# Kernel optimization log

Measured on AMD Instinct MI355X. Metric: run time of the kernel, lower is better.

Reference implementation:

```python
import jax, jax.numpy as jnp
import numpy as np

N_NODES = 100000
N_EDGES = 20000
NNZ = 1600000


def _hconv(x, node_idx, edge_idx, W, b):
    # PyG HypergraphConv (no attention): out = D^-1 H (B^-1 H^T (x W)) + b
    xw = x @ W  # [N, F_out]
    ones = jnp.ones((node_idx.shape[0],), dtype=x.dtype)
    Bdeg = jax.ops.segment_sum(ones, edge_idx, num_segments=N_EDGES)
    Binv = jnp.where(Bdeg > 0, 1.0 / Bdeg, 0.0)
    # node -> hyperedge aggregation
    e = jax.ops.segment_sum(xw[node_idx], edge_idx, num_segments=N_EDGES)
    e = e * Binv[:, None]
    Ddeg = jax.ops.segment_sum(ones, node_idx, num_segments=N_NODES)
    Dinv = jnp.where(Ddeg > 0, 1.0 / Ddeg, 0.0)
    # hyperedge -> node aggregation
    out = jax.ops.segment_sum(e[edge_idx], node_idx, num_segments=N_NODES)
    return out * Dinv[:, None] + b


def setup_inputs() -> dict:
    key = jax.random.key(0)
    ks = jax.random.split(key, 12)
    x = jax.random.normal(ks[0], (N_NODES, 300), dtype=jnp.float32)
    node_idx = jax.random.randint(ks[1], (NNZ,), 0, N_NODES)
    edge_idx = jax.random.randint(ks[2], (NNZ,), 0, N_EDGES)
    hyper_edge_index = jnp.stack([node_idx, edge_idx], axis=0)
    def lin(kw, kb, fi, fo):
        s = 1.0 / np.sqrt(fi)
        W = jax.random.uniform(kw, (fi, fo), jnp.float32, -s, s)
        b = jax.random.uniform(kb, (fo,), jnp.float32, -s, s)
        return W, b
    W1, b1 = lin(ks[3], ks[4], 300, 256)
    W2, b2 = lin(ks[5], ks[6], 256, 256)
    W3, b3 = lin(ks[7], ks[8], 256, 128)
    attn_W, attn_b = lin(ks[9], ks[10], 128, 1)
    return {"x": x, "hyper_edge_index": hyper_edge_index,
            "W1": W1, "b1": b1, "W2": W2, "b2": b2,
            "W3": W3, "b3": b3, "attn_W": attn_W, "attn_b": attn_b}


def reference(x, hyper_edge_index, W1, b1, W2, b2, W3, b3, attn_W, attn_b):
    node_idx = hyper_edge_index[0]
    edge_idx = hyper_edge_index[1]
    h = jax.nn.leaky_relu(_hconv(x, node_idx, edge_idx, W1, b1), negative_slope=0.01)
    # dropout is identity at inference
    h = jax.nn.leaky_relu(_hconv(h, node_idx, edge_idx, W2, b2), negative_slope=0.01)
    h = _hconv(h, node_idx, edge_idx, W3, b3)  # [N, 128]
    # attention pooling over all nodes (softmax along dim 0)
    logits = h @ attn_W + attn_b  # [N, 1]
    attn = jax.nn.softmax(logits, axis=0)
    return jnp.sum(attn * h, axis=0)  # [128]
```

## Files before the change

kernel.cpp:

```cpp
#include <hip/hip_runtime.h>
#include <hip/hip_bf16.h>
#include <string.h>

#define N_NODES 100000
#define N_EDGES 20000
#define NNZ     1600000

#define CHUNK   8192
#define NBE     157
#define NBN     391
#define NBLK_BIN ((NNZ + CHUNK - 1) / CHUNK)


__device__ __forceinline__ unsigned short f2bf(float f) {
    unsigned int u = __float_as_uint(f);
    unsigned int r = (u + 0x7fffu + ((u >> 16) & 1u)) >> 16;
    return (unsigned short)r;
}
__device__ __forceinline__ float bflo(unsigned int v) { return __uint_as_float(v << 16); }
__device__ __forceinline__ float bfhi(unsigned int v) { return __uint_as_float(v & 0xffff0000u); }
__device__ __forceinline__ unsigned int packbf(float lo, float hi) {
    return ((unsigned int)f2bf(hi) << 16) | (unsigned int)f2bf(lo);
}

__device__ __forceinline__ void async_copy16(const void* g, void* l) {
    __builtin_amdgcn_global_load_lds((const __attribute__((address_space(1))) void*)g,
                                     (__attribute__((address_space(3))) void*)l, 16, 0, 0);
}

typedef __attribute__((ext_vector_type(8))) short bf16x8;
typedef __attribute__((ext_vector_type(4))) float f32x4;


__global__ __launch_bounds__(256)
void hist_buckets(const int* __restrict__ node_idx, const int* __restrict__ edge_idx,
                  int* __restrict__ bcntE, int* __restrict__ bcntN) {
    __shared__ int hE[NBE];
    __shared__ int hN[NBN];
    int t = threadIdx.x;
    for (int i = t; i < NBE; i += 256) hE[i] = 0;
    for (int i = t; i < NBN; i += 256) hN[i] = 0;
    __syncthreads();
    long base = (long)blockIdx.x * CHUNK;
    #pragma unroll 4
    for (int k = 0; k < CHUNK / 256; k++) {
        long i = base + t + k * 256;
        if (i < NNZ) {
            atomicAdd(&hE[edge_idx[i] >> 7], 1);
            atomicAdd(&hN[node_idx[i] >> 8], 1);
        }
    }
    __syncthreads();
    for (int i = t; i < NBE; i += 256) if (hE[i]) atomicAdd(&bcntE[i], hE[i]);
    for (int i = t; i < NBN; i += 256) if (hN[i]) atomicAdd(&bcntN[i], hN[i]);
}

__global__ __launch_bounds__(512)
void small_scan(const int* __restrict__ cnt, int n,
                int* __restrict__ base, int* __restrict__ cursor) {
    __shared__ int tmp[512];
    int t = threadIdx.x;
    int v = (t < n) ? cnt[t] : 0;
    tmp[t] = v; __syncthreads();
    for (int s = 1; s < 512; s <<= 1) {
        int x = (t >= s) ? tmp[t - s] : 0;
        __syncthreads();
        tmp[t] += x;
        __syncthreads();
    }
    if (t < n) { int e = tmp[t] - v; base[t] = e; cursor[t] = e; }
    if (t == 0) base[n] = tmp[511];
}

__global__ __launch_bounds__(256)
void bin_pass(const int* __restrict__ key_idx, const int* __restrict__ val_idx,
              int kshift, int bshift, int nbuck,
              int* __restrict__ cursor, unsigned int* __restrict__ staged) {
    __shared__ int hist[512];
    __shared__ int gstart[512];
    int t = threadIdx.x;
    for (int i = t; i < nbuck; i += 256) hist[i] = 0;
    __syncthreads();
    long base = (long)blockIdx.x * CHUNK;
    for (int k = 0; k < CHUNK / 256; k++) {
        long i = base + t + k * 256;
        if (i < NNZ) atomicAdd(&hist[key_idx[i] >> bshift], 1);
    }
    __syncthreads();
    for (int i = t; i < nbuck; i += 256)
        gstart[i] = hist[i] ? atomicAdd(&cursor[i], hist[i]) : 0;
    __syncthreads();
    for (int i = t; i < nbuck; i += 256) hist[i] = 0;
    __syncthreads();
    for (int k = 0; k < CHUNK / 256; k++) {
        long i = base + t + k * 256;
        if (i < NNZ) {
            int key = key_idx[i], val = val_idx[i];
            int b = key >> bshift;
            int pos = gstart[b] + atomicAdd(&hist[b], 1);
            staged[pos] = ((unsigned int)key << kshift) | (unsigned int)val;
        }
    }
}

__global__ __launch_bounds__(256)
void build_csr(const unsigned int* __restrict__ staged, const int* __restrict__ bbase,
               int kshift, int bshift, int nkey,
               int* __restrict__ off, float* __restrict__ inv, int* __restrict__ csr) {
    __shared__ int cnt[256];
    __shared__ int cur[256];
    int b = blockIdx.x, t = threadIdx.x;
    int kpb = 1 << bshift;
    int key0 = b << bshift;
    unsigned int vmask = (1u << kshift) - 1u;
    if (t < kpb) cnt[t] = 0;
    __syncthreads();
    int s = bbase[b], e = bbase[b + 1];
    for (int j = s + t; j < e; j += 256)
        atomicAdd(&cnt[(int)(staged[j] >> kshift) - key0], 1);
    __syncthreads();
    int v = (t < kpb) ? cnt[t] : 0;
    cur[t] = v; __syncthreads();
    for (int st = 1; st < 256; st <<= 1) {
        int x = (t >= st) ? cur[t - st] : 0;
        __syncthreads();
        cur[t] += x;
        __syncthreads();
    }
    int excl = cur[t] - v;
    __syncthreads();
    if (t < kpb) {
        int key = key0 + t;
        if (key < nkey) {
            off[key] = s + excl;
            inv[key] = (v > 0) ? 1.0f / (float)v : 0.0f;
        }
        cur[t] = excl;
    }
    __syncthreads();
    for (int j = s + t; j < e; j += 256) {
        unsigned int pk = staged[j];
        int k = (int)(pk >> kshift) - key0;
        int pos = s + atomicAdd(&cur[k], 1);
        csr[pos] = (int)(pk & vmask);
    }
    if (b == 0 && t == 0) off[nkey] = NNZ;
}


__global__ void convert_pad_x(const float* __restrict__ x, unsigned short* __restrict__ xb) {
    int idx = blockIdx.x * 256 + threadIdx.x;
    if (idx < N_NODES * 320) {
        int r = idx / 320, k = idx - r * 320;
        xb[idx] = (k < 300) ? f2bf(x[(size_t)r * 300 + k]) : (unsigned short)0;
    }
}

__global__ void transpose_w(const float* __restrict__ W, unsigned short* __restrict__ Wt,
                            int K, int N, int Kp) {
    int n = blockIdx.x;
    for (int k = threadIdx.x; k < Kp; k += 256)
        Wt[(size_t)n * Kp + k] = (k < K) ? f2bf(W[(size_t)k * N + n]) : (unsigned short)0;
}


__global__ __launch_bounds__(256)
void gemm_bf16(const unsigned short* __restrict__ A,
               const unsigned short* __restrict__ Bt,
               unsigned short* __restrict__ C,
               int M, int Kp, int N) {
    __shared__ unsigned short As[128 * 32];
    __shared__ unsigned short Bs[128 * 32];
    int tid = threadIdx.x;
    int lane = tid & 63;
    int w = tid >> 6;
    int row0 = blockIdx.x * 128;
    int col0 = blockIdx.y * 128;
    int wm = w & 1, wn = w >> 1;

    f32x4 acc[4][4];
    #pragma unroll
    for (int i = 0; i < 4; i++)
        #pragma unroll
        for (int j = 0; j < 4; j++) acc[i][j] = (f32x4){0.f, 0.f, 0.f, 0.f};

    int sr = lane >> 2;
    int sc = lane & 3;

    for (int k0 = 0; k0 < Kp; k0 += 32) {
        #pragma unroll
        for (int c = 0; c < 2; c++) {
            int r = w * 32 + c * 16 + sr;
            int gr = row0 + r; if (gr >= M) gr = M - 1;
            const unsigned short* g = A + (size_t)gr * Kp + k0 + sc * 8;
            async_copy16(g, (void*)(As + (w * 32 + c * 16) * 32));
        }
        #pragma unroll
        for (int c = 0; c < 2; c++) {
            int r = w * 32 + c * 16 + sr;
            const unsigned short* g = Bt + (size_t)(col0 + r) * Kp + k0 + sc * 8;
            async_copy16(g, (void*)(Bs + (w * 32 + c * 16) * 32));
        }
        __syncthreads();

        bf16x8 a[4], b[4];
        #pragma unroll
        for (int i = 0; i < 4; i++)
            a[i] = *(const bf16x8*)(As + (wm * 64 + i * 16 + (lane & 15)) * 32 + (lane >> 4) * 8);
        #pragma unroll
        for (int j = 0; j < 4; j++)
            b[j] = *(const bf16x8*)(Bs + (wn * 64 + j * 16 + (lane & 15)) * 32 + (lane >> 4) * 8);
        #pragma unroll
        for (int i = 0; i < 4; i++)
            #pragma unroll
            for (int j = 0; j < 4; j++)
                acc[i][j] = __builtin_amdgcn_mfma_f32_16x16x32_bf16(a[i], b[j], acc[i][j], 0, 0, 0);
        __syncthreads();
    }

    int crow = (lane >> 4) * 4;
    int ccol = lane & 15;
    #pragma unroll
    for (int i = 0; i < 4; i++)
        #pragma unroll
        for (int r = 0; r < 4; r++) {
            int gr = row0 + wm * 64 + i * 16 + crow + r;
            if (gr < M) {
                #pragma unroll
                for (int j = 0; j < 4; j++) {
                    int gc = col0 + wn * 64 + j * 16 + ccol;
                    C[(size_t)gr * N + gc] = f2bf(acc[i][j][r]);
                }
            }
        }
}


__global__ __launch_bounds__(256)
void edge_agg256(const unsigned short* __restrict__ X, const int* __restrict__ off,
                 const int* __restrict__ csr, const float* __restrict__ inv,
                 unsigned short* __restrict__ E) {
    int wv = threadIdx.x >> 6, lane = threadIdx.x & 63;
    int seg = blockIdx.x * 4 + wv;
    if (seg >= N_EDGES) return;
    int s = off[seg], t = off[seg + 1];
    const uint2* Xp = (const uint2*)X;
    float a0 = 0.f, a1 = 0.f, a2 = 0.f, a3 = 0.f;
    int j = s;
    for (; j + 3 < t; j += 4) {
        uint2 v[4];
        #pragma unroll
        for (int q = 0; q < 4; q++) v[q] = Xp[(size_t)csr[j + q] * 64 + lane];
        #pragma unroll
        for (int q = 0; q < 4; q++) {
            a0 += bflo(v[q].x); a1 += bfhi(v[q].x);
            a2 += bflo(v[q].y); a3 += bfhi(v[q].y);
        }
    }
    for (; j < t; j++) {
        uint2 v = Xp[(size_t)csr[j] * 64 + lane];
        a0 += bflo(v.x); a1 += bfhi(v.x); a2 += bflo(v.y); a3 += bfhi(v.y);
    }
    float bi = inv[seg];
    uint2 o; o.x = packbf(a0 * bi, a1 * bi); o.y = packbf(a2 * bi, a3 * bi);
    ((uint2*)E)[(size_t)seg * 64 + lane] = o;
}

__global__ __launch_bounds__(256)
void node_agg256(const unsigned short* __restrict__ Eb, const int* __restrict__ off,
                 const int* __restrict__ csr, const float* __restrict__ inv,
                 const float* __restrict__ bias, unsigned short* __restrict__ outB) {
    int wv = threadIdx.x >> 6, lane = threadIdx.x & 63;
    int seg = blockIdx.x * 4 + wv;
    if (seg >= N_NODES) return;
    int s = off[seg], t = off[seg + 1];
    const uint2* Ep = (const uint2*)Eb;
    float a0 = 0.f, a1 = 0.f, a2 = 0.f, a3 = 0.f;
    int j = s;
    for (; j + 3 < t; j += 4) {
        uint2 v[4];
        #pragma unroll
        for (int q = 0; q < 4; q++) v[q] = Ep[(size_t)csr[j + q] * 64 + lane];
        #pragma unroll
        for (int q = 0; q < 4; q++) {
            a0 += bflo(v[q].x); a1 += bfhi(v[q].x);
            a2 += bflo(v[q].y); a3 += bfhi(v[q].y);
        }
    }
    for (; j < t; j++) {
        uint2 v = Ep[(size_t)csr[j] * 64 + lane];
        a0 += bflo(v.x); a1 += bfhi(v.x); a2 += bflo(v.y); a3 += bfhi(v.y);
    }
    float di = inv[seg];
    float4 b4 = ((const float4*)bias)[lane];
    float o0 = a0 * di + b4.x, o1 = a1 * di + b4.y;
    float o2 = a2 * di + b4.z, o3 = a3 * di + b4.w;
    o0 = (o0 > 0.f) ? o0 : 0.01f * o0;
    o1 = (o1 > 0.f) ? o1 : 0.01f * o1;
    o2 = (o2 > 0.f) ? o2 : 0.01f * o2;
    o3 = (o3 > 0.f) ? o3 : 0.01f * o3;
    uint2 o; o.x = packbf(o0, o1); o.y = packbf(o2, o3);
    ((uint2*)outB)[(size_t)seg * 64 + lane] = o;
}

__global__ __launch_bounds__(256)
void edge_agg128(const unsigned short* __restrict__ X, const int* __restrict__ off,
                 const int* __restrict__ csr, const float* __restrict__ inv,
                 unsigned short* __restrict__ E) {
    int wv = threadIdx.x >> 6, lane = threadIdx.x & 63;
    int seg = blockIdx.x * 4 + wv;
    if (seg >= N_EDGES) return;
    int s = off[seg], t = off[seg + 1];
    const unsigned int* Xp = (const unsigned int*)X;
    float a0 = 0.f, a1 = 0.f;
    int j = s;
    for (; j + 7 < t; j += 8) {
        unsigned int v[8];
        #pragma unroll
        for (int q = 0; q < 8; q++) v[q] = Xp[(size_t)csr[j + q] * 64 + lane];
        #pragma unroll
        for (int q = 0; q < 8; q++) { a0 += bflo(v[q]); a1 += bfhi(v[q]); }
    }
    for (; j < t; j++) {
        unsigned int v = Xp[(size_t)csr[j] * 64 + lane];
        a0 += bflo(v); a1 += bfhi(v);
    }
    float bi = inv[seg];
    ((unsigned int*)E)[(size_t)seg * 64 + lane] = packbf(a0 * bi, a1 * bi);
}

__global__ __launch_bounds__(256)
void node_agg128f(const unsigned short* __restrict__ Eb, const int* __restrict__ off,
                  const int* __restrict__ csr, const float* __restrict__ inv,
                  const float* __restrict__ bias, float* __restrict__ outF) {
    int wv = threadIdx.x >> 6, lane = threadIdx.x & 63;
    int seg = blockIdx.x * 4 + wv;
    if (seg >= N_NODES) return;
    int s = off[seg], t = off[seg + 1];
    const unsigned int* Ep = (const unsigned int*)Eb;
    float a0 = 0.f, a1 = 0.f;
    int j = s;
    for (; j + 7 < t; j += 8) {
        unsigned int v[8];
        #pragma unroll
        for (int q = 0; q < 8; q++) v[q] = Ep[(size_t)csr[j + q] * 64 + lane];
        #pragma unroll
        for (int q = 0; q < 8; q++) { a0 += bflo(v[q]); a1 += bfhi(v[q]); }
    }
    for (; j < t; j++) {
        unsigned int v = Ep[(size_t)csr[j] * 64 + lane];
        a0 += bflo(v); a1 += bfhi(v);
    }
    float di = inv[seg];
    float2 b2 = ((const float2*)bias)[lane];
    ((float2*)outF)[(size_t)seg * 64 + lane] = make_float2(a0 * di + b2.x, a1 * di + b2.y);
}


__global__ __launch_bounds__(256)
void logits_kernel(const float* __restrict__ H, const float* __restrict__ aW,
                   const float* __restrict__ aB, float* __restrict__ logits,
                   float* __restrict__ pmax, int N) {
    int lane = threadIdx.x & 63;
    int wave = threadIdx.x >> 6;
    int waveGlobal = blockIdx.x * 4 + wave;
    int stride = gridDim.x * 4;
    float2 w2 = ((const float2*)aW)[lane];
    float lmax = -1e30f;
    float ab = aB[0];
    for (int n = waveGlobal; n < N; n += stride) {
        float2 h2 = ((const float2*)(H + (size_t)n * 128))[lane];
        float d = h2.x * w2.x + h2.y * w2.y;
        #pragma unroll
        for (int s = 32; s > 0; s >>= 1) d += __shfl_xor(d, s, 64);
        float lg = d + ab;
        if (lane == 0) logits[n] = lg;
        lmax = fmaxf(lmax, lg);
    }
    __shared__ float wmax[4];
    if (lane == 0) wmax[wave] = lmax;
    __syncthreads();
    if (threadIdx.x == 0) {
        float m = fmaxf(fmaxf(wmax[0], wmax[1]), fmaxf(wmax[2], wmax[3]));
        pmax[blockIdx.x] = m;
    }
}

__global__ __launch_bounds__(256)
void reduce_max(const float* __restrict__ pmax, int n, float* __restrict__ gmax) {
    __shared__ float sm[256];
    float m = -1e30f;
    for (int i = threadIdx.x; i < n; i += 256) m = fmaxf(m, pmax[i]);
    sm[threadIdx.x] = m;
    __syncthreads();
    for (int s = 128; s > 0; s >>= 1) {
        if (threadIdx.x < (unsigned)s) sm[threadIdx.x] = fmaxf(sm[threadIdx.x], sm[threadIdx.x + s]);
        __syncthreads();
    }
    if (threadIdx.x == 0) *gmax = sm[0];
}

__global__ __launch_bounds__(128)
void weighted_sum(const float* __restrict__ H, const float* __restrict__ logits,
                  const float* __restrict__ gmax, float* __restrict__ gacc,
                  float* __restrict__ gsum, int N) {
    int f = threadIdx.x;
    float mx = *gmax;
    float acc = 0.f, ls = 0.f;
    for (int n = blockIdx.x; n < N; n += gridDim.x) {
        float w = __expf(logits[n] - mx);
        acc += w * H[(size_t)n * 128 + f];
        if (f == 0) ls += w;
    }
    atomicAdd(&gacc[f], acc);
    if (f == 0) atomicAdd(gsum, ls);
}

__global__ __launch_bounds__(128)
void finalize(const float* __restrict__ gacc, const float* __restrict__ gsum,
              float* __restrict__ out) {
    int f = threadIdx.x;
    out[f] = gacc[f] / gsum[0];
}


extern "C" void kernel_launch(void* const* d_in, const int* in_sizes, int n_in,
                              void* d_out, int out_size, void* d_ws, size_t ws_size,
                              hipStream_t stream) {
    const float* x        = (const float*)d_in[0];
    const int*   node_idx = (const int*)d_in[1];
    const int*   edge_idx = node_idx + NNZ;
    const float* W1 = (const float*)d_in[2];
    const float* b1 = (const float*)d_in[3];
    const float* W2 = (const float*)d_in[4];
    const float* b2 = (const float*)d_in[5];
    const float* W3 = (const float*)d_in[6];
    const float* b3 = (const float*)d_in[7];
    const float* aW = (const float*)d_in[8];
    const float* aB = (const float*)d_in[9];
    float* out = (float*)d_out;

    char* ws = (char*)d_ws;
    size_t off = 0;
    auto take = [&](size_t bytes) -> char* {
        char* r = ws + off;
        off = (off + bytes + 255) & ~(size_t)255;
        return r;
    };

    char* bcnt_base = take((size_t)(NBE + NBN) * 4);
    int* bcntE = (int*)bcnt_base;
    int* bcntN = bcntE + NBE;
    int* baseE = (int*)take((NBE + 1) * 4);
    int* baseN = (int*)take((NBN + 1) * 4);
    int* curEb = (int*)take(NBE * 4);
    int* curNb = (int*)take(NBN * 4);
    int*   offE = (int*)take((size_t)(N_EDGES + 1) * 4);
    int*   offN = (int*)take((size_t)(N_NODES + 1) * 4);
    float* Binv = (float*)take((size_t)N_EDGES * 4);
    float* Dinv = (float*)take((size_t)N_NODES * 4);
    int*   csrE = (int*)take((size_t)NNZ * 4);
    int*   csrN = (int*)take((size_t)NNZ * 4);

    unsigned short* xb  = (unsigned short*)take((size_t)N_NODES * 320 * 2);
    unsigned short* Wt1 = (unsigned short*)take((size_t)256 * 320 * 2);
    unsigned short* Wt2 = (unsigned short*)take((size_t)256 * 256 * 2);
    unsigned short* Wt3 = (unsigned short*)take((size_t)128 * 256 * 2);
    unsigned short* xw  = (unsigned short*)take((size_t)N_NODES * 256 * 2);
    unsigned short* hb  = (unsigned short*)take((size_t)N_NODES * 256 * 2);
    unsigned short* eb  = (unsigned short*)take((size_t)N_EDGES * 256 * 2);
    float* h3 = (float*)xb;

    unsigned int* stagedE = (unsigned int*)xw;
    unsigned int* stagedN = stagedE + NNZ;

    float* logits = (float*)take((size_t)N_NODES * 4);
    float* pmax   = (float*)take(400 * 4);
    char* acc_base = take((128 + 1) * 4);
    float* gacc = (float*)acc_base;
    float* gsum = gacc + 128;
    float* gmax = (float*)take(4);

    hipMemsetAsync(bcnt_base, 0, (size_t)(NBE + NBN) * 4, stream);
    hipMemsetAsync(acc_base, 0, (128 + 1) * 4, stream);

    hist_buckets<<<NBLK_BIN, 256, 0, stream>>>(node_idx, edge_idx, bcntE, bcntN);
    small_scan<<<1, 512, 0, stream>>>(bcntE, NBE, baseE, curEb);
    small_scan<<<1, 512, 0, stream>>>(bcntN, NBN, baseN, curNb);
    bin_pass<<<NBLK_BIN, 256, 0, stream>>>(edge_idx, node_idx, 17, 7, NBE, curEb, stagedE);
    bin_pass<<<NBLK_BIN, 256, 0, stream>>>(node_idx, edge_idx, 15, 8, NBN, curNb, stagedN);
    build_csr<<<NBE, 256, 0, stream>>>(stagedE, baseE, 17, 7, N_EDGES, offE, Binv, csrE);
    build_csr<<<NBN, 256, 0, stream>>>(stagedN, baseN, 15, 8, N_NODES, offN, Dinv, csrN);

    convert_pad_x<<<(N_NODES * 320 + 255) / 256, 256, 0, stream>>>(x, xb);
    transpose_w<<<256, 256, 0, stream>>>(W1, Wt1, 300, 256, 320);
    transpose_w<<<256, 256, 0, stream>>>(W2, Wt2, 256, 256, 256);
    transpose_w<<<128, 256, 0, stream>>>(W3, Wt3, 256, 128, 256);

    const int MB = (N_NODES + 127) / 128;
    const int EB = N_EDGES / 4;
    const int NB = N_NODES / 4;

    gemm_bf16<<<dim3(MB, 2), 256, 0, stream>>>(xb, Wt1, xw, N_NODES, 320, 256);
    edge_agg256<<<EB, 256, 0, stream>>>(xw, offE, csrE, Binv, eb);
    node_agg256<<<NB, 256, 0, stream>>>(eb, offN, csrN, Dinv, b1, hb);

    gemm_bf16<<<dim3(MB, 2), 256, 0, stream>>>(hb, Wt2, xw, N_NODES, 256, 256);
    edge_agg256<<<EB, 256, 0, stream>>>(xw, offE, csrE, Binv, eb);
    node_agg256<<<NB, 256, 0, stream>>>(eb, offN, csrN, Dinv, b2, hb);

    gemm_bf16<<<dim3(MB, 1), 256, 0, stream>>>(hb, Wt3, xw, N_NODES, 256, 128);
    edge_agg128<<<EB, 256, 0, stream>>>(xw, offE, csrE, Binv, eb);
    node_agg128f<<<NB, 256, 0, stream>>>(eb, offN, csrN, Dinv, b3, h3);

    logits_kernel<<<400, 256, 0, stream>>>(h3, aW, aB, logits, pmax, N_NODES);
    reduce_max<<<1, 256, 0, stream>>>(pmax, 400, gmax);
    weighted_sum<<<512, 128, 0, stream>>>(h3, logits, gmax, gacc, gsum, N_NODES);
    finalize<<<1, 128, 0, stream>>>(gacc, gsum, out);
}
```

Measured before the change: 1.048 ms.

## Aggregate node features to hyperedges before the linear transform

```diff
diff --git a/kernel.cpp b/kernel.cpp
--- a/kernel.cpp
+++ b/kernel.cpp
@@ -237,6 +237,46 @@
 
 
 __global__ __launch_bounds__(256)
+void edge_agg320(const unsigned short* __restrict__ X, const int* __restrict__ off,
+                 const int* __restrict__ csr, const float* __restrict__ inv,
+                 unsigned short* __restrict__ E) {
+    int wv = threadIdx.x >> 6, lane = threadIdx.x & 63;
+    int seg = blockIdx.x * 4 + wv;
+    if (seg >= N_EDGES) return;
+    int s = off[seg], t = off[seg + 1];
+    const uint2* Xp = (const uint2*)X;
+    const unsigned int* Xu = (const unsigned int*)X;
+    bool ex = (lane < 32);
+    float a0 = 0.f, a1 = 0.f, a2 = 0.f, a3 = 0.f, a4 = 0.f, a5 = 0.f;
+    int j = s;
+    for (; j + 3 < t; j += 4) {
+        uint2 v[4]; unsigned int w[4];
+        #pragma unroll
+        for (int q = 0; q < 4; q++) {
+            size_t r = (size_t)csr[j + q];
+            v[q] = Xp[r * 80 + lane];
+            if (ex) w[q] = Xu[r * 160 + 128 + lane];
+        }
+        #pragma unroll
+        for (int q = 0; q < 4; q++) {
+            a0 += bflo(v[q].x); a1 += bfhi(v[q].x);
+            a2 += bflo(v[q].y); a3 += bfhi(v[q].y);
+            if (ex) { a4 += bflo(w[q]); a5 += bfhi(w[q]); }
+        }
+    }
+    for (; j < t; j++) {
+        size_t r = (size_t)csr[j];
+        uint2 v = Xp[r * 80 + lane];
+        a0 += bflo(v.x); a1 += bfhi(v.x); a2 += bflo(v.y); a3 += bfhi(v.y);
+        if (ex) { unsigned int w = Xu[r * 160 + 128 + lane]; a4 += bflo(w); a5 += bfhi(w); }
+    }
+    float bi = inv[seg];
+    uint2 o; o.x = packbf(a0 * bi, a1 * bi); o.y = packbf(a2 * bi, a3 * bi);
+    ((uint2*)E)[(size_t)seg * 80 + lane] = o;
+    if (ex) ((unsigned int*)E)[(size_t)seg * 160 + 128 + lane] = packbf(a4 * bi, a5 * bi);
+}
+
+__global__ __launch_bounds__(256)
 void edge_agg256(const unsigned short* __restrict__ X, const int* __restrict__ off,
                  const int* __restrict__ csr, const float* __restrict__ inv,
                  unsigned short* __restrict__ E) {
@@ -247,12 +287,12 @@
     const uint2* Xp = (const uint2*)X;
     float a0 = 0.f, a1 = 0.f, a2 = 0.f, a3 = 0.f;
     int j = s;
-    for (; j + 3 < t; j += 4) {
-        uint2 v[4];
-        #pragma unroll
-        for (int q = 0; q < 4; q++) v[q] = Xp[(size_t)csr[j + q] * 64 + lane];
-        #pragma unroll
-        for (int q = 0; q < 4; q++) {
+    for (; j + 7 < t; j += 8) {
+        uint2 v[8];
+        #pragma unroll
+        for (int q = 0; q < 8; q++) v[q] = Xp[(size_t)csr[j + q] * 64 + lane];
+        #pragma unroll
+        for (int q = 0; q < 8; q++) {
             a0 += bflo(v[q].x); a1 += bfhi(v[q].x);
             a2 += bflo(v[q].y); a3 += bfhi(v[q].y);
         }
@@ -277,12 +317,12 @@
     const uint2* Ep = (const uint2*)Eb;
     float a0 = 0.f, a1 = 0.f, a2 = 0.f, a3 = 0.f;
     int j = s;
-    for (; j + 3 < t; j += 4) {
-        uint2 v[4];
-        #pragma unroll
-        for (int q = 0; q < 4; q++) v[q] = Ep[(size_t)csr[j + q] * 64 + lane];
-        #pragma unroll
-        for (int q = 0; q < 4; q++) {
+    for (; j + 7 < t; j += 8) {
+        uint2 v[8];
+        #pragma unroll
+        for (int q = 0; q < 8; q++) v[q] = Ep[(size_t)csr[j + q] * 64 + lane];
+        #pragma unroll
+        for (int q = 0; q < 8; q++) {
             a0 += bflo(v[q].x); a1 += bfhi(v[q].x);
             a2 += bflo(v[q].y); a3 += bfhi(v[q].y);
         }
@@ -301,32 +341,6 @@
     o3 = (o3 > 0.f) ? o3 : 0.01f * o3;
     uint2 o; o.x = packbf(o0, o1); o.y = packbf(o2, o3);
     ((uint2*)outB)[(size_t)seg * 64 + lane] = o;
-}
-
-__global__ __launch_bounds__(256)
-void edge_agg128(const unsigned short* __restrict__ X, const int* __restrict__ off,
-                 const int* __restrict__ csr, const float* __restrict__ inv,
-                 unsigned short* __restrict__ E) {
-    int wv = threadIdx.x >> 6, lane = threadIdx.x & 63;
-    int seg = blockIdx.x * 4 + wv;
-    if (seg >= N_EDGES) return;
-    int s = off[seg], t = off[seg + 1];
-    const unsigned int* Xp = (const unsigned int*)X;
-    float a0 = 0.f, a1 = 0.f;
-    int j = s;
-    for (; j + 7 < t; j += 8) {
-        unsigned int v[8];
-        #pragma unroll
-        for (int q = 0; q < 8; q++) v[q] = Xp[(size_t)csr[j + q] * 64 + lane];
-        #pragma unroll
-        for (int q = 0; q < 8; q++) { a0 += bflo(v[q]); a1 += bfhi(v[q]); }
-    }
-    for (; j < t; j++) {
-        unsigned int v = Xp[(size_t)csr[j] * 64 + lane];
-        a0 += bflo(v); a1 += bfhi(v);
-    }
-    float bi = inv[seg];
-    ((unsigned int*)E)[(size_t)seg * 64 + lane] = packbf(a0 * bi, a1 * bi);
 }
 
 __global__ __launch_bounds__(256)
@@ -466,12 +480,12 @@
     unsigned short* Wt1 = (unsigned short*)take((size_t)256 * 320 * 2);
     unsigned short* Wt2 = (unsigned short*)take((size_t)256 * 256 * 2);
     unsigned short* Wt3 = (unsigned short*)take((size_t)128 * 256 * 2);
-    unsigned short* xw  = (unsigned short*)take((size_t)N_NODES * 256 * 2);
-    unsigned short* hb  = (unsigned short*)take((size_t)N_NODES * 256 * 2);
-    unsigned short* eb  = (unsigned short*)take((size_t)N_EDGES * 256 * 2);
+    unsigned short* eagg = (unsigned short*)take((size_t)N_EDGES * 320 * 2);
+    unsigned short* eb   = (unsigned short*)take((size_t)N_EDGES * 256 * 2);
+    unsigned short* hb   = (unsigned short*)take((size_t)N_NODES * 256 * 2);
     float* h3 = (float*)xb;
 
-    unsigned int* stagedE = (unsigned int*)xw;
+    unsigned int* stagedE = (unsigned int*)hb;
     unsigned int* stagedN = stagedE + NNZ;
 
     float* logits = (float*)take((size_t)N_NODES * 4);
@@ -497,20 +511,20 @@
     transpose_w<<<256, 256, 0, stream>>>(W2, Wt2, 256, 256, 256);
     transpose_w<<<128, 256, 0, stream>>>(W3, Wt3, 256, 128, 256);
 
-    const int MB = (N_NODES + 127) / 128;
+    const int ME = (N_EDGES + 127) / 128;
     const int EB = N_EDGES / 4;
     const int NB = N_NODES / 4;
 
-    gemm_bf16<<<dim3(MB, 2), 256, 0, stream>>>(xb, Wt1, xw, N_NODES, 320, 256);
-    edge_agg256<<<EB, 256, 0, stream>>>(xw, offE, csrE, Binv, eb);
+    edge_agg320<<<EB, 256, 0, stream>>>(xb, offE, csrE, Binv, eagg);
+    gemm_bf16<<<dim3(ME, 2), 256, 0, stream>>>(eagg, Wt1, eb, N_EDGES, 320, 256);
     node_agg256<<<NB, 256, 0, stream>>>(eb, offN, csrN, Dinv, b1, hb);
 
-    gemm_bf16<<<dim3(MB, 2), 256, 0, stream>>>(hb, Wt2, xw, N_NODES, 256, 256);
-    edge_agg256<<<EB, 256, 0, stream>>>(xw, offE, csrE, Binv, eb);
+    edge_agg256<<<EB, 256, 0, stream>>>(hb, offE, csrE, Binv, eagg);
+    gemm_bf16<<<dim3(ME, 2), 256, 0, stream>>>(eagg, Wt2, eb, N_EDGES, 256, 256);
     node_agg256<<<NB, 256, 0, stream>>>(eb, offN, csrN, Dinv, b2, hb);
 
-    gemm_bf16<<<dim3(MB, 1), 256, 0, stream>>>(hb, Wt3, xw, N_NODES, 256, 128);
-    edge_agg128<<<EB, 256, 0, stream>>>(xw, offE, csrE, Binv, eb);
+    edge_agg256<<<EB, 256, 0, stream>>>(hb, offE, csrE, Binv, eagg);
+    gemm_bf16<<<dim3(ME, 1), 256, 0, stream>>>(eagg, Wt3, eb, N_EDGES, 256, 128);
     node_agg128f<<<NB, 256, 0, stream>>>(eb, offN, csrN, Dinv, b3, h3);
 
     logits_kernel<<<400, 256, 0, stream>>>(h3, aW, aB, logits, pmax, N_NODES);
```

New measurement: 1.096 ms. 4.6% more time.
